# Optimization experiments

Hardware: AMD Instinct MI355X
Metric: run time of the kernel (lower is better)

Reference implementation:

```python
import jax, jax.numpy as jnp
import numpy as np

HEAD_NUM = 16

def setup_inputs() -> dict:
    key = jax.random.key(0)
    k1, k2 = jax.random.split(key)
    bs, seq, d = 2, 2048, 1024
    embeddings = jax.random.normal(k1, (bs, seq, d), dtype=jnp.float32)
    W = jax.random.normal(k2, (d, 3 * d), dtype=jnp.float32) * (1.0 / np.sqrt(d))
    b = jnp.zeros((3 * d,), dtype=jnp.float32)
    return {"embeddings": embeddings, "W": W, "b": b}

def reference(embeddings, W, b):
    bs, seq, d = embeddings.shape
    h = HEAD_NUM
    qkv = embeddings @ W + b                      # [b, s, 3d]
    q, k, v = jnp.split(qkv, 3, axis=-1)          # each [b, s, d]
    hd = d // h
    # Faithful to source: reshape to (bs, seq, head_dim, heads) then permute
    def split_heads(x, head_dim):
        return x.reshape(bs, seq, head_dim, h).transpose(0, 3, 1, 2)  # [b, h, s, hd]
    mq = split_heads(q, hd)
    mk = split_heads(k, hd)
    mv = split_heads(v, hd)
    scale = jnp.sqrt(jnp.asarray(hd, dtype=mq.dtype))
    scores = jnp.einsum('bhqd,bhkd->bhqk', mq, mk) / scale  # [b, h, s, s]
    attn = jax.nn.softmax(scores, axis=-1)
    out = jnp.einsum('bhqk,bhkv->bhqv', attn, mv)            # [b, h, s, hd]
    return out.transpose(0, 2, 1, 3).reshape(bs, seq, -1)    # [b, s, d]
```

## Files before the change

kernel.cpp:

```cpp
#include <hip/hip_runtime.h>
#include <stdint.h>

typedef unsigned short u16;
typedef unsigned int u32;
typedef unsigned int u32x2 __attribute__((ext_vector_type(2)));
typedef float f32x4 __attribute__((ext_vector_type(4)));
typedef __bf16 bf16x8 __attribute__((ext_vector_type(8)));

#define BS 2
#define SEQ 2048
#define DIM 1024
#define NW3 3072
#define NH 16
#define HD 64

#define MFMA_BF16(a, b, c) __builtin_amdgcn_mfma_f32_16x16x32_bf16((a), (b), (c), 0, 0, 0)

#define GLL16(g, l)                                                                \
  __builtin_amdgcn_global_load_lds(                                                \
      (__attribute__((address_space(1))) void*)(void*)(uintptr_t)(g),              \
      (__attribute__((address_space(3))) void*)(l), 16, 0, 0)

__device__ __forceinline__ float fexp2(float x) {
#if defined(__has_builtin)
#if __has_builtin(__builtin_amdgcn_exp2f)
  return __builtin_amdgcn_exp2f(x);
#else
  return exp2f(x);
#endif
#else
  return exp2f(x);
#endif
}

__device__ __forceinline__ u16 f2bf(float x) {
  __bf16 h = (__bf16)x;
  return __builtin_bit_cast(u16, h);
}

#define CSC 0.18033688011112042f

#if defined(__has_builtin)
#if __has_builtin(__builtin_amdgcn_permlane32_swap) && \
    __has_builtin(__builtin_amdgcn_permlane16_swap)
#define HAVE_PLSWAP 1
#endif
#endif

__device__ __forceinline__ uint4 p_transform(u32 pk00, u32 pk01, u32 pk10, u32 pk11,
                                             int sl0, int sl1, bool hi) {
#ifdef HAVE_PLSWAP
  u32x2 s0 = __builtin_amdgcn_permlane32_swap(pk00, pk10, false, false);
  u32x2 s1 = __builtin_amdgcn_permlane32_swap(pk01, pk11, false, false);
  u32x2 t0 = __builtin_amdgcn_permlane16_swap(s0[0], s0[1], false, false);
  u32x2 t1 = __builtin_amdgcn_permlane16_swap(s1[0], s1[1], false, false);
  uint4 wv;
  wv.x = t0[0]; wv.y = t1[0]; wv.z = t0[1]; wv.w = t1[1];
  return wv;
#else
  u32 a0 = __shfl(pk00, sl0), a1 = __shfl(pk01, sl0);
  u32 a2 = __shfl(pk00, sl1), a3 = __shfl(pk01, sl1);
  u32 b0 = __shfl(pk10, sl0), b1 = __shfl(pk11, sl0);
  u32 b2 = __shfl(pk10, sl1), b3 = __shfl(pk11, sl1);
  uint4 wv;
  wv.x = hi ? b0 : a0; wv.y = hi ? b1 : a1;
  wv.z = hi ? b2 : a2; wv.w = hi ? b3 : a3;
  return wv;
#endif
}

__global__ __launch_bounds__(256) void conv_kernel(const float* __restrict__ A,
                                                   u16* __restrict__ O,
                                                   const float* __restrict__ W,
                                                   u16* __restrict__ Wt) {
  if (blockIdx.x < 4096) {
    int i = (blockIdx.x * 256 + threadIdx.x) * 4;
    float4 v = *(const float4*)(A + i);
    union { u16 u[4]; ushort4 v4; } p;
    p.u[0] = f2bf(v.x); p.u[1] = f2bf(v.y); p.u[2] = f2bf(v.z); p.u[3] = f2bf(v.w);
    *(ushort4*)(O + i) = p.v4;
  } else {
    __shared__ __align__(16) u16 lt[64][68];
    int b2 = blockIdx.x - 4096;
    int ktile = b2 / 48, ntile = b2 - ktile * 48;
    int k0 = ktile * 64, n0 = ntile * 64;
    int rowb = threadIdx.x >> 4, c4 = (threadIdx.x & 15) * 4;
#pragma unroll
    for (int rr = 0; rr < 4; ++rr) {
      int row = rowb + rr * 16;
      float4 v = *(const float4*)(W + (size_t)(k0 + row) * NW3 + n0 + c4);
      union { u16 u[4]; uint2 d; } pk;
      pk.u[0] = f2bf(v.x); pk.u[1] = f2bf(v.y); pk.u[2] = f2bf(v.z); pk.u[3] = f2bf(v.w);
      *(uint2*)&lt[row][c4] = pk.d;
    }
    __syncthreads();
    int j = threadIdx.x >> 2, seg = threadIdx.x & 3;
    int n = n0 + j;
    int h = n & 15, hd = (n & 1023) >> 4;
    int np = (n & ~1023) + h * 64 + hd;
    union { u16 u[16]; uint4 q[2]; } o;
#pragma unroll
    for (int idx = 0; idx < 16; ++idx) o.u[idx] = lt[seg * 16 + idx][j];
    u16* dst = Wt + (size_t)np * DIM + k0 + seg * 16;
    *(uint4*)(dst) = o.q[0];
    *(uint4*)(dst + 8) = o.q[1];
  }
}

#define GSTAGE(ADST, BDST, KT)                                                 \
  {                                                                            \
    const int koff = (KT) * 64;                                \
    _Pragma("unroll") for (int r = 0; r < 2; ++r) {                            \
      int l = r * 256 + t;                            \
      int row = l >> 2, pos = l & 3;                                           \
      int kc = pos ^ (row & 3);                                                \
      GLL16(Abase + row * 2048 + koff + kc * 16, (char*)(ADST) + l * 16);      \
      GLL16(Bbase + row * 2048 + koff + kc * 16, (char*)(BDST) + l * 16);      \
    }                                                                          \
  }

#define GCOMPUTE(AT, BT)                                                       \
  {                                                                            \
    bf16x8 af[4], bfr[4];                                                      \
    _Pragma("unroll") for (int mt = 0; mt < 4; ++mt) {                         \
      int row = wm + mt * 16 + c;                                              \
      int kc = quad ^ (row & 3);                                               \
      af[mt] = *(const bf16x8*)((const char*)(AT) + row * 64 + kc * 16);       \
    }                                                                          \
    _Pragma("unroll") for (int nt = 0; nt < 4; ++nt) {                         \
      int row = wn + nt * 16 + c;                                              \
      int kc = quad ^ (row & 3);                                               \
      bfr[nt] = *(const bf16x8*)((const char*)(BT) + row * 64 + kc * 16);      \
    }                                                                          \
    _Pragma("unroll") for (int mt = 0; mt < 4; ++mt)                           \
      _Pragma("unroll") for (int nt = 0; nt < 4; ++nt)                         \
        acc[mt][nt] = MFMA_BF16(af[mt], bfr[nt], acc[mt][nt]);                 \
  }

__global__ __launch_bounds__(256) void gemm_qkv_kernel(
    const u16* __restrict__ Ab, const u16* __restrict__ Bt, const float* __restrict__ bias,
    u16* __restrict__ Q, u16* __restrict__ K, u16* __restrict__ Vt) {
  __shared__ __align__(16) u16 Aa[128 * 32];
  __shared__ __align__(16) u16 Ab2[128 * 32];
  __shared__ __align__(16) u16 Ba[128 * 32];
  __shared__ __align__(16) u16 Bb2[128 * 32];
  const int t = threadIdx.x;
  const int lane = t & 63, wave = t >> 6;
  const int c = lane & 15, quad = lane >> 4;
  const int wid = (blockIdx.x & 7) * 96 + (blockIdx.x >> 3);
  const int tm = wid / 24, tn = wid - tm * 24;
  const int wm = (wave >> 1) * 64, wn = (wave & 1) * 64;

  const char* Abase = (const char*)(Ab + (size_t)tm * 128 * DIM);
  const char* Bbase = (const char*)(Bt + (size_t)tn * 128 * DIM);

  f32x4 z = {0.f, 0.f, 0.f, 0.f};
  f32x4 acc[4][4];
#pragma unroll
  for (int i = 0; i < 4; ++i)
#pragma unroll
    for (int j = 0; j < 4; ++j) acc[i][j] = z;

  GSTAGE(Aa, Ba, 0);
  __syncthreads();
  for (int kt = 0; kt < 32; kt += 2) {
    GSTAGE(Ab2, Bb2, kt + 1);
    GCOMPUTE(Aa, Ba);
    __syncthreads();
    if (kt + 2 < 32) GSTAGE(Aa, Ba, kt + 2);
    GCOMPUTE(Ab2, Bb2);
    __syncthreads();
  }

#pragma unroll
  for (int nt = 0; nt < 4; ++nt) {
    int np = tn * 128 + wn + nt * 16 + c;
    int which = np >> 10;
    int rem = np & 1023;
    int h = rem >> 6, hd = rem & 63;
    float bv = bias[(np & ~1023) + hd * 16 + h];
    float sc = (which == 0) ? CSC : 1.0f;
    float bvs = bv * sc;
#pragma unroll
    for (int mt = 0; mt < 4; ++mt) {
      int mbase = tm * 128 + wm + mt * 16 + quad * 4;
      int bI = mbase >> 11;
      int s0 = mbase & 2047;
      if (which == 2) {
        union { u16 u[4]; uint2 v; } p;
#pragma unroll
        for (int r = 0; r < 4; ++r) p.u[r] = f2bf(acc[mt][nt][r] + bv);
        *(uint2*)(Vt + ((size_t)(bI * NH + h) * HD + hd) * SEQ + s0) = p.v;
      } else {
        u16* dst = (which == 0) ? Q : K;
#pragma unroll
        for (int r = 0; r < 4; ++r)
          dst[((size_t)(bI * NH + h) * SEQ + (s0 + r)) * HD + hd] =
              f2bf(acc[mt][nt][r] * sc + bvs);
      }
    }
  }
}

#define STAGE_KV(KDST, VDST, KTILE)                                            \
  {                                                                            \
    const char* Ktb = Kb + (size_t)(KTILE) * 8192;        \
    const char* Vtb = Vb + (size_t)(KTILE) * 128;         \
    _Pragma("unroll") for (int r = 0; r < 2; ++r) {                            \
      int l = r * 256 + t;                                                     \
      int row = l >> 3, pos = l & 7;                                           \
      int kc = pos ^ (row & 7);                                                \
      GLL16(Ktb + row * 128 + kc * 16, (char*)(KDST) + l * 16);                \
      GLL16(Vtb + row * 4096 + kc * 16, (char*)(VDST) + l * 16);               \
    }                                                                          \
  }

#define COMPUTE_TILE(KT, VT)                                                   \
  {                                                                            \
    f32x4 sT[2][2]; \
    sT[0][0] = z; sT[0][1] = z; sT[1][0] = z; sT[1][1] = z;                    \
    __builtin_amdgcn_s_setprio(1);                                             \
    _Pragma("unroll") for (int mt2 = 0; mt2 < 2; ++mt2) {                      \
      _Pragma("unroll") for (int ks = 0; ks < 2; ++ks) {                       \
        int row = ws * 32 + mt2 * 16 + c;                                      \
        int kc = (ks * 4 + quad) ^ (row & 7);                                  \
        bf16x8 kf = *(const bf16x8*)((const char*)(KT) + row * 128 + kc * 16); \
        sT[mt2][0] = MFMA_BF16(kf, qf[0][ks], sT[mt2][0]);                     \
        sT[mt2][1] = MFMA_BF16(kf, qf[1][ks], sT[mt2][1]);                     \
      }                                                                        \
    }                                                                          \
    __builtin_amdgcn_s_setprio(0);                                             \
    bf16x8 pf[2];                                                              \
    _Pragma("unroll") for (int nt = 0; nt < 2; ++nt) {                         \
      u32 pk[2][2];                                                            \
      _Pragma("unroll") for (int mt2 = 0; mt2 < 2; ++mt2) {                    \
        float p0 = fexp2(sT[mt2][nt][0]);                                      \
        float p1 = fexp2(sT[mt2][nt][1]);                                      \
        float p2 = fexp2(sT[mt2][nt][2]);                                      \
        float p3 = fexp2(sT[mt2][nt][3]);                                      \
        pk[mt2][0] = (u32)f2bf(p0) | ((u32)f2bf(p1) << 16);                    \
        pk[mt2][1] = (u32)f2bf(p2) | ((u32)f2bf(p3) << 16);                    \
      }                                                                        \
      uint4 wv = p_transform(pk[0][0], pk[0][1], pk[1][0], pk[1][1],           \
                             sl0, sl1, hi);                                    \
      pf[nt] = __builtin_bit_cast(bf16x8, wv);                                 \
    }                                                                          \
    __builtin_amdgcn_s_setprio(1);                                             \
    _Pragma("unroll") for (int mt = 0; mt < 4; ++mt) {                         \
      int row = mt * 16 + c;                                                   \
      int kc = vq ^ (row & 7);                                                 \
      bf16x8 vf = *(const bf16x8*)((const char*)(VT) + row * 128 + kc * 16);   \
      accO[mt][0] = MFMA_BF16(vf, pf[0], accO[mt][0]);                         \
      accO[mt][1] = MFMA_BF16(vf, pf[1], accO[mt][1]);                         \
    }                                                                          \
    acc_l[0] = MFMA_BF16(ones, pf[0], acc_l[0]);   \
    acc_l[1] = MFMA_BF16(ones, pf[1], acc_l[1]);                               \
    __builtin_amdgcn_s_setprio(0);                                             \
  }

__global__ __launch_bounds__(256, 4) void attn_kernel(
    const u16* __restrict__ Q, const u16* __restrict__ K,
    const u16* __restrict__ Vt, float* __restrict__ Out) {
  __shared__ __align__(16) u16 Ka[64 * 64];
  __shared__ __align__(16) u16 Kb2[64 * 64];
  __shared__ __align__(16) u16 Va[64 * 64];
  __shared__ __align__(16) u16 Vb2[64 * 64];
  const int t = threadIdx.x;
  const int lane = t & 63, wave = t >> 6;
  const int c = lane & 15, quad = lane >> 4;
  const int wq = wave & 1, ws = wave >> 1;
  const int p = blockIdx.x;
  const int xcd = p & 7, slot = p >> 3;
  const int bh = xcd + ((slot >> 5) << 3);
  const int qt = slot & 31;
  const int h = bh & 15, b = bh >> 4;

  const u16* Qb = Q + ((size_t)bh * SEQ + qt * 64) * HD;
  const char* Kb = (const char*)(K + (size_t)bh * SEQ * HD);
  const char* Vb = (const char*)(Vt + (size_t)bh * HD * SEQ);

#pragma unroll
  for (int r = 0; r < 2; ++r) {
    int l = r * 256 + t;
    int row = l >> 3, pos = l & 7;
    int kc = pos ^ (row & 7);
    GLL16((const char*)Qb + row * 128 + kc * 16, (char*)Ka + l * 16);
  }
  __syncthreads();
  bf16x8 qf[2][2];
#pragma unroll
  for (int nt = 0; nt < 2; ++nt)
#pragma unroll
    for (int ks = 0; ks < 2; ++ks) {
      int row = wq * 32 + nt * 16 + c;
      int kc = (ks * 4 + quad) ^ (row & 7);
      qf[nt][ks] = *(const bf16x8*)((const char*)Ka + row * 128 + kc * 16);
    }
  __syncthreads();

  f32x4 z = {0.f, 0.f, 0.f, 0.f};
  f32x4 accO[4][2];
#pragma unroll
  for (int i = 0; i < 4; ++i) { accO[i][0] = z; accO[i][1] = z; }
  f32x4 acc_l[2] = {z, z};
  const uint4 onesw = {0x3F803F80u, 0x3F803F80u, 0x3F803F80u, 0x3F803F80u};
  const bf16x8 ones = __builtin_bit_cast(bf16x8, onesw);

  const int sl0 = c + 16 * ((quad & 1) * 2);
  const int sl1 = sl0 + 16;
  const bool hi = quad >= 2;
  const int vq = ws * 4 + quad;

  STAGE_KV(Ka, Va, 0);
  __syncthreads();

  for (int kt = 0; kt < 32; kt += 2) {
    STAGE_KV(Kb2, Vb2, kt + 1);
    COMPUTE_TILE(Ka, Va);
    __syncthreads();
    if (kt + 2 < 32) STAGE_KV(Ka, Va, kt + 2);
    COMPUTE_TILE(Kb2, Vb2);
    __syncthreads();
  }

  float sm[2];
  sm[0] = acc_l[0][0];
  sm[1] = acc_l[1][0];
  if (ws == 1) {
    float* fb = (float*)(wq ? (void*)Kb2 : (void*)Ka);
#pragma unroll
    for (int mt = 0; mt < 4; ++mt)
#pragma unroll
      for (int nt = 0; nt < 2; ++nt)
        *(f32x4*)(fb + (mt * 2 + nt) * 256 + lane * 4) = accO[mt][nt];
    float* lb = (float*)Va + wq * 128;
    lb[lane * 2] = sm[0];
    lb[lane * 2 + 1] = sm[1];
  }
  __syncthreads();
  if (ws == 0) {
    const float* fb = (const float*)(wq ? (void*)Kb2 : (void*)Ka);
#pragma unroll
    for (int mt = 0; mt < 4; ++mt)
#pragma unroll
      for (int nt = 0; nt < 2; ++nt)
        accO[mt][nt] += *(const f32x4*)(fb + (mt * 2 + nt) * 256 + lane * 4);
    const float* lb = (const float*)Va + wq * 128;
    float inv0 = 1.f / (sm[0] + lb[lane * 2]);
    float inv1 = 1.f / (sm[1] + lb[lane * 2 + 1]);
    int s0 = qt * 64 + wq * 32 + c;
#pragma unroll
    for (int mt = 0; mt < 4; ++mt) {
#pragma unroll
      for (int nt = 0; nt < 2; ++nt) {
        float inv = nt ? inv1 : inv0;
        float4 o;
        o.x = accO[mt][nt][0] * inv;
        o.y = accO[mt][nt][1] * inv;
        o.z = accO[mt][nt][2] * inv;
        o.w = accO[mt][nt][3] * inv;
        size_t off = ((size_t)(b * SEQ + s0 + nt * 16)) * DIM + h * HD + mt * 16 + quad * 4;
        *(float4*)(Out + off) = o;
      }
    }
  }
}

extern "C" void kernel_launch(void* const* d_in, const int* in_sizes, int n_in,
                              void* d_out, int out_size, void* d_ws, size_t ws_size,
                              hipStream_t stream) {
  (void)in_sizes; (void)n_in; (void)out_size; (void)ws_size;
  const float* emb = (const float*)d_in[0];
  const float* W = (const float*)d_in[1];
  const float* bias = (const float*)d_in[2];
  float* out = (float*)d_out;
  char* ws = (char*)d_ws;
  u16* Ab = (u16*)ws;
  u16* Wt = (u16*)(ws + 8388608);
  u16* Qd = (u16*)(ws + 14680064);
  u16* Kd = (u16*)(ws + 23068672);
  u16* Vd = (u16*)(ws + 31457280);

  conv_kernel<<<4864, 256, 0, stream>>>(emb, Ab, W, Wt);
  gemm_qkv_kernel<<<768, 256, 0, stream>>>(Ab, Wt, bias, Qd, Kd, Vd);
  attn_kernel<<<1024, 256, 0, stream>>>(Qd, Kd, Vd, out);
}
```

Before: 159.7 us.

## Triple-buffer QKV GEMM LDS stages with partial vmcnt waits

Moves the QKV projection GEMM from double to triple buffering in LDS. Two k-tiles are prefetched ahead, and each iteration waits with a partial s_waitcnt vmcnt(4) plus a raw s_barrier instead of a full __syncthreads. The aim is to hide global-to-LDS load latency behind the MFMA work. It raises LDS use from 32KB to 48KB per block, which may reduce occupancy, and it relies on every GSTAGE issuing exactly 4 loads per thread.

```diff
diff --git a/kernel.cpp b/kernel.cpp
--- a/kernel.cpp
+++ b/kernel.cpp
@@ -140,10 +140,12 @@
 __global__ __launch_bounds__(256) void gemm_qkv_kernel(
     const u16* __restrict__ Ab, const u16* __restrict__ Bt, const float* __restrict__ bias,
     u16* __restrict__ Q, u16* __restrict__ K, u16* __restrict__ Vt) {
-  __shared__ __align__(16) u16 Aa[128 * 32];
-  __shared__ __align__(16) u16 Ab2[128 * 32];
-  __shared__ __align__(16) u16 Ba[128 * 32];
-  __shared__ __align__(16) u16 Bb2[128 * 32];
+  __shared__ __align__(16) u16 A0[128 * 32];
+  __shared__ __align__(16) u16 A1[128 * 32];
+  __shared__ __align__(16) u16 A2[128 * 32];
+  __shared__ __align__(16) u16 B0[128 * 32];
+  __shared__ __align__(16) u16 B1[128 * 32];
+  __shared__ __align__(16) u16 B2[128 * 32];
   const int t = threadIdx.x;
   const int lane = t & 63, wave = t >> 6;
   const int c = lane & 15, quad = lane >> 4;
@@ -161,15 +163,28 @@
 #pragma unroll
     for (int j = 0; j < 4; ++j) acc[i][j] = z;
 
-  GSTAGE(Aa, Ba, 0);
-  __syncthreads();
-  for (int kt = 0; kt < 32; kt += 2) {
-    GSTAGE(Ab2, Bb2, kt + 1);
-    GCOMPUTE(Aa, Ba);
-    __syncthreads();
-    if (kt + 2 < 32) GSTAGE(Aa, Ba, kt + 2);
-    GCOMPUTE(Ab2, Bb2);
-    __syncthreads();
+  GSTAGE(A0, B0, 0);
+  GSTAGE(A1, B1, 1);
+  asm volatile("s_waitcnt vmcnt(4)" ::: "memory");
+  __builtin_amdgcn_s_barrier();
+  __builtin_amdgcn_sched_barrier(0);
+
+  const u16 *pa = A0, *pb = B0;
+  const u16 *qa = A1, *qb = B1;
+  const u16 *ra = A2, *rb = B2;
+#pragma unroll 1
+  for (int kt = 0; kt < 32; ++kt) {
+    if (kt + 2 < 32) GSTAGE(ra, rb, kt + 2);
+    GCOMPUTE(pa, pb);
+    if (kt + 2 < 32) {
+      asm volatile("s_waitcnt vmcnt(4)" ::: "memory");
+    } else {
+      asm volatile("s_waitcnt vmcnt(0)" ::: "memory");
+    }
+    __builtin_amdgcn_s_barrier();
+    __builtin_amdgcn_sched_barrier(0);
+    const u16* ta = pa; pa = qa; qa = ra; ra = ta;
+    const u16* tb = pb; pb = qb; qb = rb; rb = tb;
   }
 
 #pragma unroll
```

After: 160.2 us. No clear change (+0.3%).
